# Performance work log

Hardware: AMD Instinct MI355X
Metric: run time of the kernel (lower is better)

The kernel has to match this reference:

```python
import jax, jax.numpy as jnp
import numpy as np

# static sizes
B = 32          # graphs
NPER = 1024     # nodes per graph
N0 = B * NPER
F_IN = 128
H = 4           # heads
DH = 32         # per-head dim (128/4)
HID = H * DH    # 128
E = 524288      # edges (avg degree 16)
K1, K2, K3 = 512, 256, 128  # ceil(0.5*nper) per stage
NC = 10


def gcn_agg(h, src, dst, w, n):
    """GCNConv propagation: sym-normalized aggregation with self-loops.
    h: [n,F] already projected; w: [E] edge weight (0 for filtered edges)."""
    deg = jax.ops.segment_sum(w, dst, num_segments=n) + 1.0  # +1 self-loop
    dinv = jax.lax.rsqrt(deg)
    coef = dinv[src] * dinv[dst] * w                          # [E]
    agg = jax.ops.segment_sum(h[src] * coef[:, None], dst, num_segments=n)
    return agg + h / deg[:, None]  # self-loop term: dinv[i]^2 = 1/deg[i]


def mh_gcn(x, W, b, src, dst, w, n):
    """MAGPoolGCNLayer: per-head GCNConv (32->32), relu, concat heads."""
    h = jnp.einsum('nhd,hde->nhe', x.reshape(n, H, DH), W).reshape(n, HID)
    return jax.nn.relu(gcn_agg(h, src, dst, w, n) + b.reshape(HID))


def att_pool(x, src, dst, w, A, psW, psb, n, k):
    """MultiHeadAtt: standard att, complex score, concat pooling, global weight."""
    sub = x.reshape(n, H, DH)
    att = jnp.einsum('nhd,hd->nh', sub, A)            # per-head Linear(32,1)
    cat = (att[:, :, None] * sub).reshape(n, HID)     # score*sub, concat
    score = (gcn_agg(cat @ psW, src, dst, w, n) + psb)[:, 0]  # GCNConv(HID,1)
    nper = n // B
    _, idx = jax.lax.top_k(score.reshape(B, nper), k)  # per-graph topk
    perm = (idx + jnp.arange(B)[:, None] * nper).reshape(-1)
    xn = x[perm] * jnp.tanh(score[perm])[:, None]      # global att weighting
    # filter_adj: remap kept nodes, mask edges touching dropped nodes
    nmap = jnp.full((n,), -1, jnp.int32).at[perm].set(jnp.arange(B * k, dtype=jnp.int32))
    ns, nd = nmap[src], nmap[dst]
    wn = w * ((ns >= 0) & (nd >= 0)).astype(w.dtype)
    return xn, jnp.maximum(ns, 0), jnp.maximum(nd, 0), wn


def readout(x):
    # graphs are contiguous with equal node counts -> reshape readout
    xr = x.reshape(B, -1, x.shape[-1])
    return jnp.concatenate([xr.max(1), xr.mean(1)], axis=1)  # [B, 2*HID]


def setup_inputs():
    key = jax.random.key(0)
    ks = jax.random.split(key, 26)
    gid = jnp.repeat(jnp.arange(B, dtype=jnp.int32), E // B)
    src = jax.random.randint(ks[0], (E,), 0, NPER, dtype=jnp.int32) + gid * NPER
    dst = jax.random.randint(ks[1], (E,), 0, NPER, dtype=jnp.int32) + gid * NPER
    x = jax.random.normal(ks[2], (N0, F_IN), jnp.float32)
    s = 0.1
    def rn(k, shp):
        return jax.random.normal(k, shp, jnp.float32) * s
    return {
        'x': x, 'src': src, 'dst': dst,
        'W1': rn(ks[3], (H, DH, DH)), 'b1': rn(ks[4], (H, DH)), 'A1': rn(ks[5], (H, DH)),
        'ps1W': rn(ks[6], (HID, 1)), 'ps1b': rn(ks[7], (1,)),
        'W2': rn(ks[8], (H, DH, DH)), 'b2': rn(ks[9], (H, DH)), 'A2': rn(ks[10], (H, DH)),
        'ps2W': rn(ks[11], (HID, 1)), 'ps2b': rn(ks[12], (1,)),
        'W3': rn(ks[13], (H, DH, DH)), 'b3': rn(ks[14], (H, DH)), 'A3': rn(ks[15], (H, DH)),
        'ps3W': rn(ks[16], (HID, 1)), 'ps3b': rn(ks[17], (1,)),
        'l1W': rn(ks[18], (2 * HID, HID)), 'l1b': rn(ks[19], (HID,)),
        'l2W': rn(ks[20], (HID, HID // 2)), 'l2b': rn(ks[21], (HID // 2,)),
        'l3W': rn(ks[22], (HID // 2, NC)), 'l3b': rn(ks[23], (NC,)),
    }


def reference(x, src, dst, W1, b1, A1, ps1W, ps1b, W2, b2, A2, ps2W, ps2b,
              W3, b3, A3, ps3W, ps3b, l1W, l1b, l2W, l2b, l3W, l3b):
    w = jnp.ones((E,), x.dtype)
    h = mh_gcn(x, W1, b1, src, dst, w, N0)
    h, s1, d1, w1 = att_pool(h, src, dst, w, A1, ps1W, ps1b, N0, K1)
    r1 = readout(h)
    n1 = B * K1
    h = mh_gcn(h, W2, b2, s1, d1, w1, n1)
    h, s2, d2, w2 = att_pool(h, s1, d1, w1, A2, ps2W, ps2b, n1, K2)
    r2 = readout(h)
    n2 = B * K2
    h = mh_gcn(h, W3, b3, s2, d2, w2, n2)
    h, _, _, _ = att_pool(h, s2, d2, w2, A3, ps3W, ps3b, n2, K3)
    r3 = readout(h)
    z = r1 + r2 + r3                      # [B, 2*HID]
    z = jax.nn.relu(z @ l1W + l1b)        # dropout skipped (eval mode)
    z = jax.nn.relu(z @ l2W + l2b)
    return jax.nn.log_softmax(z @ l3W + l3b, axis=-1)
```

## Files before the change

### kernel.cpp

```cpp
#include <hip/hip_runtime.h>
#include <math.h>

#define BGR 32
#define NPER0 1024
#define N0 (BGR * NPER0)
#define FDIM 128
#define EDG 524288
#define EPG (EDG / BGR)
#define EBLK (EDG / 256)
#define K1 512
#define K2 256
#define K3 128
#define N1 (BGR * K1)
#define N2 (BGR * K2)
#define SXP 36
#define CAP 64
#define RSEC (BGR * FDIM)

__device__ __forceinline__ unsigned enc_f(float v) {
    unsigned u = __float_as_uint(v);
    return (u & 0x80000000u) ? ~u : (u | 0x80000000u);
}
__device__ __forceinline__ float dec_f(unsigned u) {
    return (u & 0x80000000u) ? __uint_as_float(u ^ 0x80000000u) : __uint_as_float(~u);
}

__device__ __forceinline__ void proj_compute(float* __restrict__ hp, int nb, int t,
                                             const float* __restrict__ sW,
                                             const float* __restrict__ sxT) {
    const int fg = t >> 3, ng = t & 7, h = fg >> 3;
    const float* ap = sxT + h * 32 * SXP + ng * 4;
    const float* bp = sW + h * 1024 + (fg & 7) * 4;
    float4 acc0 = {0.f, 0.f, 0.f, 0.f}, acc1 = acc0, acc2 = acc0, acc3 = acc0;
#pragma unroll
    for (int k = 0; k < 32; k++) {
        float4 a = *(const float4*)(ap + k * SXP);
        float4 b = *(const float4*)(bp + k * 32);
        acc0.x = fmaf(a.x, b.x, acc0.x); acc0.y = fmaf(a.x, b.y, acc0.y);
        acc0.z = fmaf(a.x, b.z, acc0.z); acc0.w = fmaf(a.x, b.w, acc0.w);
        acc1.x = fmaf(a.y, b.x, acc1.x); acc1.y = fmaf(a.y, b.y, acc1.y);
        acc1.z = fmaf(a.y, b.z, acc1.z); acc1.w = fmaf(a.y, b.w, acc1.w);
        acc2.x = fmaf(a.z, b.x, acc2.x); acc2.y = fmaf(a.z, b.y, acc2.y);
        acc2.z = fmaf(a.z, b.z, acc2.z); acc2.w = fmaf(a.z, b.w, acc2.w);
        acc3.x = fmaf(a.w, b.x, acc3.x); acc3.y = fmaf(a.w, b.y, acc3.y);
        acc3.z = fmaf(a.w, b.z, acc3.z); acc3.w = fmaf(a.w, b.w, acc3.w);
    }
    float4* op = (float4*)(hp + (size_t)(nb + ng * 4) * FDIM + fg * 4);
    op[0] = acc0; op[32] = acc1; op[64] = acc2; op[96] = acc3;
}

__device__ __forceinline__ void pool_body(const float* __restrict__ ha,
                                          const int* __restrict__ perm,
                                          const float* __restrict__ mult, int k, int pb,
                                          unsigned* __restrict__ rmax,
                                          float* __restrict__ rsum,
                                          float* __restrict__ smax,
                                          float* __restrict__ ssum) {
    const int t = threadIdx.x;
    const int g = pb & 31;
    const int c = pb >> 5;
    const int f = t & 127, half = t >> 7;
    const int base = g * k + c * 8;
    float vmax = -1e30f, vsum = 0.0f;
#pragma unroll
    for (int j0 = 0; j0 < 4; j0++) {
        int newid = base + half + j0 * 2;
        int old = perm[newid];
        float m = mult[newid];
        float v = ha[(size_t)old * FDIM + f] * m;
        vmax = fmaxf(vmax, v);
        vsum += v;
    }
    if (half) { smax[f] = vmax; ssum[f] = vsum; }
    __syncthreads();
    if (!half) {
        vmax = fmaxf(vmax, smax[f]);
        vsum += ssum[f];
        atomicMax(&rmax[g * FDIM + f], enc_f(vmax));
        atomicAdd(&rsum[g * FDIM + f], vsum);
    }
}

__global__ void bin_proj1(const int* __restrict__ src, const int* __restrict__ dst,
                          int* __restrict__ cnt, int* __restrict__ slot,
                          const float* __restrict__ x, const float* __restrict__ W,
                          float* __restrict__ hp,
                          unsigned* __restrict__ rmax, float* __restrict__ rsum) {
    __shared__ __align__(16) float sW[4096];
    __shared__ __align__(16) float sxT[128 * SXP];
    const int t = threadIdx.x;
    if (blockIdx.x < EBLK) {
        if (blockIdx.x < BGR) {
            int z = blockIdx.x * 256 + t;
            rmax[z] = 0u;
            rsum[z] = 0.0f;
        }
        const int g = blockIdx.x & 31, chunk = blockIdx.x >> 5;
        int e = g * EPG + chunk * 256 + t;
        int s = src[e];
        int d = dst[e];
        int p = atomicAdd(&cnt[d], 1);
        if (p < CAP) slot[(size_t)d * CAP + p] = s;
        return;
    }
    const int tb = blockIdx.x - EBLK;
    const int nb = (tb & 31) * NPER0 + (tb >> 5) * 32;
    for (int i = t; i < 4096; i += 256) sW[i] = W[i];
    for (int i = t; i < 4096; i += 256) {
        int node = i >> 7, dim = i & 127;
        sxT[dim * SXP + node] = x[(size_t)(nb + node) * FDIM + dim];
    }
    __syncthreads();
    proj_compute(hp, nb, t, sW, sxT);
}

__global__ void comp_proj_pool(const int* __restrict__ cnt_prev,
                               const int* __restrict__ slot_prev,
                               const int* __restrict__ nmap,
                               int* __restrict__ cnt_next, int* __restrict__ slot_next,
                               const float* __restrict__ ha, const int* __restrict__ perm,
                               const float* __restrict__ mult, const float* __restrict__ W,
                               float* __restrict__ hp, int ncomp, int ntiles, int kprev,
                               unsigned* __restrict__ rmax, float* __restrict__ rsum) {
    __shared__ __align__(16) float sW[4096];
    __shared__ __align__(16) float sxT[128 * SXP];
    const int t = threadIdx.x;
    if (blockIdx.x < ncomp) {
        const int w = t >> 6, lane = t & 63;
        const int b = (blockIdx.x & 31) * kprev + (blockIdx.x >> 5) * 4 + w;
        const int old = perm[b];
        const int c = min(cnt_prev[old], CAP);
        int a = -1;
        if (lane < c) a = nmap[slot_prev[(size_t)old * CAP + lane]];
        unsigned long long mk = __ballot(a >= 0);
        if (a >= 0) {
            int pos = __popcll(mk & ((1ull << lane) - 1ull));
            slot_next[(size_t)b * CAP + pos] = a;
        }
        if (lane == 0) cnt_next[b] = __popcll(mk);
        return;
    }
    if (blockIdx.x >= ncomp + ntiles) {
        pool_body(ha, perm, mult, kprev, blockIdx.x - (ncomp + ntiles), rmax, rsum,
                  sW, sW + 128);
        return;
    }
    const int tb = blockIdx.x - ncomp;
    const int nb = (tb & 31) * kprev + (tb >> 5) * 32;
    for (int i = t; i < 4096; i += 256) sW[i] = W[i];
    for (int i = t; i < 4096; i += 256) {
        int node = i >> 7, dim = i & 127;
        int newid = nb + node;
        sxT[dim * SXP + node] = ha[(size_t)perm[newid] * FDIM + dim] * mult[newid];
    }
    __syncthreads();
    proj_compute(hp, nb, t, sW, sxT);
}

__global__ void agg_kernel(const float* __restrict__ hp, const float* __restrict__ b,
                           const int* __restrict__ cnt, const int* __restrict__ slot,
                           const float* __restrict__ A, const float* __restrict__ psW,
                           float* __restrict__ ha, float* __restrict__ csd, int nper) {
    const int w = threadIdx.x >> 6;
    const int lane = threadIdx.x & 63;
    const int g = blockIdx.x & 31;
    const int chunk = blockIdx.x >> 5;
    const int i = g * nper + chunk * 4 + w;
    const int ci = cnt[i];
    const float di = rsqrtf((float)ci + 1.0f);
    const int c = min(ci, CAP);
    const float2* __restrict__ hp2 = (const float2*)hp;
    float2 self = hp2[(size_t)i * 64 + lane];
    float accx = self.x * di * di, accy = self.y * di * di;
    int idx = 0;
    float dv = 0.0f;
    if (lane < c) {
        idx = slot[i * CAP + lane];
        dv = rsqrtf((float)cnt[idx] + 1.0f);
    }
    int j = 0;
    for (; j + 3 < c; j += 4) {
        int s0 = __shfl(idx, j, 64);
        int s1 = __shfl(idx, j + 1, 64);
        int s2 = __shfl(idx, j + 2, 64);
        int s3 = __shfl(idx, j + 3, 64);
        float c0 = __shfl(dv, j, 64) * di;
        float c1 = __shfl(dv, j + 1, 64) * di;
        float c2 = __shfl(dv, j + 2, 64) * di;
        float c3 = __shfl(dv, j + 3, 64) * di;
        float2 v0 = hp2[(size_t)s0 * 64 + lane];
        float2 v1 = hp2[(size_t)s1 * 64 + lane];
        float2 v2 = hp2[(size_t)s2 * 64 + lane];
        float2 v3 = hp2[(size_t)s3 * 64 + lane];
        accx = fmaf(v0.x, c0, accx); accy = fmaf(v0.y, c0, accy);
        accx = fmaf(v1.x, c1, accx); accy = fmaf(v1.y, c1, accy);
        accx = fmaf(v2.x, c2, accx); accy = fmaf(v2.y, c2, accy);
        accx = fmaf(v3.x, c3, accx); accy = fmaf(v3.y, c3, accy);
    }
    for (; j < c; j++) {
        int s = __shfl(idx, j, 64);
        float co = __shfl(dv, j, 64) * di;
        float2 v = hp2[(size_t)s * 64 + lane];
        accx = fmaf(v.x, co, accx); accy = fmaf(v.y, co, accy);
    }
    float2 bb = ((const float2*)b)[lane];
    float2 o;
    o.x = fmaxf(accx + bb.x, 0.0f);
    o.y = fmaxf(accy + bb.y, 0.0f);
    ((float2*)ha)[(size_t)i * 64 + lane] = o;
    float2 Av = ((const float2*)A)[lane];
    float2 Pv = ((const float2*)psW)[lane];
    float a = o.x * Av.x + o.y * Av.y;
    float p = o.x * Pv.x + o.y * Pv.y;
#pragma unroll
    for (int d = 8; d > 0; d >>= 1) {
        a += __shfl_down(a, d, 16);
        p += __shfl_down(p, d, 16);
    }
    float part = a * p;
    part += __shfl_down(part, 16, 64);
    part += __shfl_down(part, 32, 64);
    if (lane == 0) csd[i] = part * di;
}

__global__ __launch_bounds__(1024) void topk_kernel(
        const float* __restrict__ csd, const int* __restrict__ cnt,
        const int* __restrict__ slot, const float* __restrict__ psb,
        int nper, int k, int* __restrict__ nmap, int* __restrict__ perm,
        float* __restrict__ mult) {
    __shared__ float cs_l[NPER0];
    __shared__ float sc[NPER0];
    __shared__ unsigned ukey[NPER0];
    __shared__ unsigned hist[256];
    __shared__ unsigned wtot[4];
    __shared__ unsigned sel[2];
    __shared__ int ctr[2];
    const int g = blockIdx.x, t = threadIdx.x;
    const int gnb = g * nper;
    if (t < nper) cs_l[t] = csd[gnb + t];
    if (t == 0) { sel[0] = 0u; sel[1] = (unsigned)k; }
    __syncthreads();
    if (t < nper) {
        int ci = cnt[gnb + t];
        int c = min(ci, CAP);
        const int* srow = slot + (size_t)(gnb + t) * CAP;
        float v = 0.0f;
        for (int j = 0; j < c; j++) v += cs_l[srow[j] - gnb];
        float s = rsqrtf((float)ci + 1.0f) * (v + cs_l[t]) + psb[0];
        sc[t] = s;
        ukey[t] = enc_f(s);
    }
    __syncthreads();
    const int w4 = t >> 6, l = t & 63;
    for (int shift = 24; shift >= 0; shift -= 8) {
        if (t < 256) hist[t] = 0u;
        __syncthreads();
        const unsigned prefix = sel[0];
        const unsigned need = sel[1];
        {
            unsigned u = (t < nper) ? ukey[t] : 0u;
            bool inp = (t < nper) &&
                       ((shift == 24) || ((u >> (shift + 8)) == (prefix >> (shift + 8))));
            int dig = inp ? (int)((u >> shift) & 255u) : -1;
            int cv = inp ? 1 : 0;
#pragma unroll
            for (int d = 1; d < 64; d <<= 1) {
                int od = __shfl_xor(dig, d, 64);
                int oc = __shfl_xor(cv, d, 64);
                if (od == dig) cv = ((l & d) == 0) ? (cv + oc) : 0;
            }
            if (dig >= 0 && cv > 0) atomicAdd(&hist[dig], (unsigned)cv);
        }
        __syncthreads();
        unsigned h = 0, s = 0;
        if (t < 256) {
            h = hist[t];
            s = h;
#pragma unroll
            for (int off = 1; off < 64; off <<= 1) {
                unsigned v2 = __shfl_down(s, off, 64);
                if (l + off < 64) s += v2;
            }
            if (l == 0) wtot[w4] = s;
        }
        __syncthreads();
        if (t < 256) {
            unsigned add = 0;
            for (int ww = w4 + 1; ww < 4; ww++) add += wtot[ww];
            const unsigned sfx = s + add;
            const unsigned gtr = sfx - h;
            if (sfx >= need && gtr < need) {
                sel[0] = prefix | ((unsigned)t << shift);
                sel[1] = need - gtr;
            }
        }
        __syncthreads();
    }
    const unsigned T = sel[0];
    const int need2 = (int)sel[1];
    if (t == 0) { ctr[0] = 0; ctr[1] = k - need2; }
    __syncthreads();
    if (t < nper) {
        unsigned u = ukey[t];
        int newid = -1;
        if (u > T) {
            newid = atomicAdd(&ctr[0], 1);
        } else if (u == T) {
            int s2 = atomicAdd(&ctr[1], 1);
            if (s2 < k) newid = s2;
        }
        nmap[gnb + t] = (newid >= 0) ? g * k + newid : -1;
        if (newid >= 0) {
            perm[g * k + newid] = gnb + t;
            mult[g * k + newid] = tanhf(sc[t]);
        }
    }
}

__global__ __launch_bounds__(1024) void pool3_mlp(
        const float* __restrict__ ha, const int* __restrict__ perm,
        const float* __restrict__ mult,
        const unsigned* __restrict__ rmax, const float* __restrict__ rsum,
        const float* __restrict__ l1W, const float* __restrict__ l1b,
        const float* __restrict__ l2W, const float* __restrict__ l2b,
        const float* __restrict__ l3W, const float* __restrict__ l3b,
        float* __restrict__ out) {
    __shared__ float pm[8][FDIM], ps[8][FDIM];
    __shared__ float sz[256], s1[128], s2[64], s3[16], red[2];
    const int g = blockIdx.x, t = threadIdx.x;
    const int f = t & 127, ch = t >> 7;
    float vmax = -1e30f, vsum = 0.0f;
#pragma unroll
    for (int j = 0; j < K3 / 8; j++) {
        int nid = g * K3 + ch + j * 8;
        int old = perm[nid];
        float m = mult[nid];
        float v = ha[(size_t)old * FDIM + f] * m;
        vmax = fmaxf(vmax, v);
        vsum += v;
    }
    pm[ch][f] = vmax;
    ps[ch][f] = vsum;
    __syncthreads();
    if (t < 128) {
        float M = pm[0][t];
#pragma unroll
        for (int c2 = 1; c2 < 8; c2++) M = fmaxf(M, pm[c2][t]);
        sz[t] = dec_f(rmax[g * FDIM + t]) + dec_f(rmax[RSEC + g * FDIM + t]) + M;
    } else if (t < 256) {
        int f2 = t - 128;
        float S = ps[0][f2];
#pragma unroll
        for (int c2 = 1; c2 < 8; c2++) S += ps[c2][f2];
        sz[t] = rsum[g * FDIM + f2] / (float)K1 + rsum[RSEC + g * FDIM + f2] / (float)K2 +
                S / (float)K3;
    }
    __syncthreads();
    if (t < 128) {
        float acc = l1b[t];
        for (int i = 0; i < 256; i++) acc = fmaf(sz[i], l1W[i * 128 + t], acc);
        s1[t] = fmaxf(acc, 0.0f);
    }
    __syncthreads();
    if (t < 64) {
        float a2 = l2b[t];
        for (int i = 0; i < 128; i++) a2 = fmaf(s1[i], l2W[i * 64 + t], a2);
        s2[t] = fmaxf(a2, 0.0f);
    }
    __syncthreads();
    if (t < 10) {
        float a3 = l3b[t];
        for (int i = 0; i < 64; i++) a3 = fmaf(s2[i], l3W[i * 10 + t], a3);
        s3[t] = a3;
    }
    __syncthreads();
    if (t == 0) {
        float m = -1e30f;
        for (int c = 0; c < 10; c++) m = fmaxf(m, s3[c]);
        float sum = 0.0f;
        for (int c = 0; c < 10; c++) sum += expf(s3[c] - m);
        red[0] = m;
        red[1] = logf(sum);
    }
    __syncthreads();
    if (t < 10) out[g * 10 + t] = s3[t] - red[0] - red[1];
}

extern "C" void kernel_launch(void* const* d_in, const int* in_sizes, int n_in,
                              void* d_out, int out_size, void* d_ws, size_t ws_size,
                              hipStream_t stream) {
    const float* x    = (const float*)d_in[0];
    const int* src0   = (const int*)d_in[1];
    const int* dst0   = (const int*)d_in[2];
    const float* W1   = (const float*)d_in[3];
    const float* b1   = (const float*)d_in[4];
    const float* A1   = (const float*)d_in[5];
    const float* ps1W = (const float*)d_in[6];
    const float* ps1b = (const float*)d_in[7];
    const float* W2   = (const float*)d_in[8];
    const float* b2   = (const float*)d_in[9];
    const float* A2   = (const float*)d_in[10];
    const float* ps2W = (const float*)d_in[11];
    const float* ps2b = (const float*)d_in[12];
    const float* W3   = (const float*)d_in[13];
    const float* b3   = (const float*)d_in[14];
    const float* A3   = (const float*)d_in[15];
    const float* ps3W = (const float*)d_in[16];
    const float* ps3b = (const float*)d_in[17];
    const float* l1W  = (const float*)d_in[18];
    const float* l1b  = (const float*)d_in[19];
    const float* l2W  = (const float*)d_in[20];
    const float* l2b  = (const float*)d_in[21];
    const float* l3W  = (const float*)d_in[22];
    const float* l3b  = (const float*)d_in[23];
    float* out = (float*)d_out;

    char* ws = (char*)d_ws;
    size_t o = 0;
    auto alloc = [&](size_t bytes) -> void* {
        void* p = ws + o;
        o += (bytes + 255) & ~(size_t)255;
        return p;
    };
    float*    hproj = (float*)alloc((size_t)N0 * FDIM * 4);
    float*    hact  = (float*)alloc((size_t)N0 * FDIM * 4);
    int*      cntA  = (int*)alloc(N0 * 4);
    int*      cntB  = (int*)alloc(N1 * 4);
    int*      cntC  = (int*)alloc(N2 * 4);
    int*      slotA = (int*)alloc((size_t)N0 * CAP * 4);
    int*      slotB = (int*)alloc((size_t)N1 * CAP * 4);
    int*      slotC = (int*)alloc((size_t)N2 * CAP * 4);
    float*    cs    = (float*)alloc(N0 * 4);
    int*      nmapA = (int*)alloc(N0 * 4);
    int*      nmapB = (int*)alloc(N1 * 4);
    int*      perm  = (int*)alloc(N1 * 4);
    float*    mult  = (float*)alloc(N1 * 4);
    unsigned* rmax  = (unsigned*)alloc(2 * RSEC * 4);
    float*    rsum  = (float*)alloc(2 * RSEC * 4);

    hipMemsetAsync(cntA, 0, N0 * 4, stream);
    bin_proj1<<<EBLK + N0 / 32, 256, 0, stream>>>(src0, dst0, cntA, slotA, x, W1,
                                                  hproj, rmax, rsum);
    agg_kernel<<<N0 / 4, 256, 0, stream>>>(hproj, b1, cntA, slotA, A1, ps1W, hact, cs, NPER0);
    topk_kernel<<<BGR, 1024, 0, stream>>>(cs, cntA, slotA, ps1b, NPER0, K1,
                                          nmapA, perm, mult);

    comp_proj_pool<<<N1 / 4 + N1 / 32 + BGR * K1 / 8, 256, 0, stream>>>(
        cntA, slotA, nmapA, cntB, slotB, hact, perm, mult, W2, hproj,
        N1 / 4, N1 / 32, K1, rmax, rsum);
    agg_kernel<<<N1 / 4, 256, 0, stream>>>(hproj, b2, cntB, slotB, A2, ps2W, hact, cs, K1);
    topk_kernel<<<BGR, 1024, 0, stream>>>(cs, cntB, slotB, ps2b, K1, K2,
                                          nmapB, perm, mult);

    comp_proj_pool<<<N2 / 4 + N2 / 32 + BGR * K2 / 8, 256, 0, stream>>>(
        cntB, slotB, nmapB, cntC, slotC, hact, perm, mult, W3, hproj,
        N2 / 4, N2 / 32, K2, rmax + RSEC, rsum + RSEC);
    agg_kernel<<<N2 / 4, 256, 0, stream>>>(hproj, b3, cntC, slotC, A3, ps3W, hact, cs, K2);
    topk_kernel<<<BGR, 1024, 0, stream>>>(cs, cntC, slotC, ps3b, K2, K3,
                                          nmapA , perm, mult);

    pool3_mlp<<<BGR, 1024, 0, stream>>>(hact, perm, mult, rmax, rsum,
                                        l1W, l1b, l2W, l2b, l3W, l3b, out);

    (void)in_sizes; (void)n_in; (void)out_size; (void)ws_size;
}
```

Baseline: 247.6 us.

## Aggregate before projecting and fold compaction and pooling into top-k kernel

Uses linearity to run the sparse GCN aggregation on raw features first, then applies the per-head 32x32 projection inside the aggregation kernel. This removes the separate projection pass and its intermediate buffer. Edge compaction, readout pooling and the final MLP now run inside a per-graph top-k kernel with a shared-memory node map, which removes global atomics and several launches. The trade-off is that each aggregation block reloads the 16KB weight matrix, and compaction and pooling now run on only 32 blocks, so there is less parallelism.

```diff
diff --git a/kernel.cpp b/kernel.cpp
--- a/kernel.cpp
+++ b/kernel.cpp
@@ -13,7 +13,6 @@
 #define K3 128
 #define N1 (BGR * K1)
 #define N2 (BGR * K2)
-#define SXP 36
 #define CAP 64
 #define RSEC (BGR * FDIM)
 
@@ -21,193 +20,98 @@
     unsigned u = __float_as_uint(v);
     return (u & 0x80000000u) ? ~u : (u | 0x80000000u);
 }
-__device__ __forceinline__ float dec_f(unsigned u) {
-    return (u & 0x80000000u) ? __uint_as_float(u ^ 0x80000000u) : __uint_as_float(~u);
-}
-
-__device__ __forceinline__ void proj_compute(float* __restrict__ hp, int nb, int t,
-                                             const float* __restrict__ sW,
-                                             const float* __restrict__ sxT) {
-    const int fg = t >> 3, ng = t & 7, h = fg >> 3;
-    const float* ap = sxT + h * 32 * SXP + ng * 4;
-    const float* bp = sW + h * 1024 + (fg & 7) * 4;
-    float4 acc0 = {0.f, 0.f, 0.f, 0.f}, acc1 = acc0, acc2 = acc0, acc3 = acc0;
-#pragma unroll
-    for (int k = 0; k < 32; k++) {
-        float4 a = *(const float4*)(ap + k * SXP);
-        float4 b = *(const float4*)(bp + k * 32);
-        acc0.x = fmaf(a.x, b.x, acc0.x); acc0.y = fmaf(a.x, b.y, acc0.y);
-        acc0.z = fmaf(a.x, b.z, acc0.z); acc0.w = fmaf(a.x, b.w, acc0.w);
-        acc1.x = fmaf(a.y, b.x, acc1.x); acc1.y = fmaf(a.y, b.y, acc1.y);
-        acc1.z = fmaf(a.y, b.z, acc1.z); acc1.w = fmaf(a.y, b.w, acc1.w);
-        acc2.x = fmaf(a.z, b.x, acc2.x); acc2.y = fmaf(a.z, b.y, acc2.y);
-        acc2.z = fmaf(a.z, b.z, acc2.z); acc2.w = fmaf(a.z, b.w, acc2.w);
-        acc3.x = fmaf(a.w, b.x, acc3.x); acc3.y = fmaf(a.w, b.y, acc3.y);
-        acc3.z = fmaf(a.w, b.z, acc3.z); acc3.w = fmaf(a.w, b.w, acc3.w);
-    }
-    float4* op = (float4*)(hp + (size_t)(nb + ng * 4) * FDIM + fg * 4);
-    op[0] = acc0; op[32] = acc1; op[64] = acc2; op[96] = acc3;
-}
-
-__device__ __forceinline__ void pool_body(const float* __restrict__ ha,
-                                          const int* __restrict__ perm,
-                                          const float* __restrict__ mult, int k, int pb,
-                                          unsigned* __restrict__ rmax,
-                                          float* __restrict__ rsum,
-                                          float* __restrict__ smax,
-                                          float* __restrict__ ssum) {
+
+__global__ void bin_kernel(const int* __restrict__ src, const int* __restrict__ dst,
+                           int* __restrict__ cnt, int* __restrict__ slot) {
+    const int g = blockIdx.x & 31, chunk = blockIdx.x >> 5;
+    int e = g * EPG + chunk * 256 + threadIdx.x;
+    int s = src[e];
+    int d = dst[e];
+    int p = atomicAdd(&cnt[d], 1);
+    if (p < CAP) slot[(size_t)d * CAP + p] = s;
+}
+
+__global__ void aggw_kernel(const float* __restrict__ xsrc,
+                            const int* __restrict__ permIn,
+                            const float* __restrict__ multIn,
+                            const int* __restrict__ cnt, const int* __restrict__ slot,
+                            const float* __restrict__ W, const float* __restrict__ b,
+                            const float* __restrict__ A, const float* __restrict__ psW,
+                            float* __restrict__ haOut, float* __restrict__ csd,
+                            int nper) {
+    __shared__ __align__(16) float sW[4096];
+    __shared__ float sY[4][128];
     const int t = threadIdx.x;
-    const int g = pb & 31;
-    const int c = pb >> 5;
-    const int f = t & 127, half = t >> 7;
-    const int base = g * k + c * 8;
-    float vmax = -1e30f, vsum = 0.0f;
-#pragma unroll
-    for (int j0 = 0; j0 < 4; j0++) {
-        int newid = base + half + j0 * 2;
-        int old = perm[newid];
-        float m = mult[newid];
-        float v = ha[(size_t)old * FDIM + f] * m;
-        vmax = fmaxf(vmax, v);
-        vsum += v;
-    }
-    if (half) { smax[f] = vmax; ssum[f] = vsum; }
-    __syncthreads();
-    if (!half) {
-        vmax = fmaxf(vmax, smax[f]);
-        vsum += ssum[f];
-        atomicMax(&rmax[g * FDIM + f], enc_f(vmax));
-        atomicAdd(&rsum[g * FDIM + f], vsum);
-    }
-}
-
-__global__ void bin_proj1(const int* __restrict__ src, const int* __restrict__ dst,
-                          int* __restrict__ cnt, int* __restrict__ slot,
-                          const float* __restrict__ x, const float* __restrict__ W,
-                          float* __restrict__ hp,
-                          unsigned* __restrict__ rmax, float* __restrict__ rsum) {
-    __shared__ __align__(16) float sW[4096];
-    __shared__ __align__(16) float sxT[128 * SXP];
-    const int t = threadIdx.x;
-    if (blockIdx.x < EBLK) {
-        if (blockIdx.x < BGR) {
-            int z = blockIdx.x * 256 + t;
-            rmax[z] = 0u;
-            rsum[z] = 0.0f;
-        }
-        const int g = blockIdx.x & 31, chunk = blockIdx.x >> 5;
-        int e = g * EPG + chunk * 256 + t;
-        int s = src[e];
-        int d = dst[e];
-        int p = atomicAdd(&cnt[d], 1);
-        if (p < CAP) slot[(size_t)d * CAP + p] = s;
-        return;
-    }
-    const int tb = blockIdx.x - EBLK;
-    const int nb = (tb & 31) * NPER0 + (tb >> 5) * 32;
-    for (int i = t; i < 4096; i += 256) sW[i] = W[i];
-    for (int i = t; i < 4096; i += 256) {
-        int node = i >> 7, dim = i & 127;
-        sxT[dim * SXP + node] = x[(size_t)(nb + node) * FDIM + dim];
-    }
-    __syncthreads();
-    proj_compute(hp, nb, t, sW, sxT);
-}
-
-__global__ void comp_proj_pool(const int* __restrict__ cnt_prev,
-                               const int* __restrict__ slot_prev,
-                               const int* __restrict__ nmap,
-                               int* __restrict__ cnt_next, int* __restrict__ slot_next,
-                               const float* __restrict__ ha, const int* __restrict__ perm,
-                               const float* __restrict__ mult, const float* __restrict__ W,
-                               float* __restrict__ hp, int ncomp, int ntiles, int kprev,
-                               unsigned* __restrict__ rmax, float* __restrict__ rsum) {
-    __shared__ __align__(16) float sW[4096];
-    __shared__ __align__(16) float sxT[128 * SXP];
-    const int t = threadIdx.x;
-    if (blockIdx.x < ncomp) {
-        const int w = t >> 6, lane = t & 63;
-        const int b = (blockIdx.x & 31) * kprev + (blockIdx.x >> 5) * 4 + w;
-        const int old = perm[b];
-        const int c = min(cnt_prev[old], CAP);
-        int a = -1;
-        if (lane < c) a = nmap[slot_prev[(size_t)old * CAP + lane]];
-        unsigned long long mk = __ballot(a >= 0);
-        if (a >= 0) {
-            int pos = __popcll(mk & ((1ull << lane) - 1ull));
-            slot_next[(size_t)b * CAP + pos] = a;
-        }
-        if (lane == 0) cnt_next[b] = __popcll(mk);
-        return;
-    }
-    if (blockIdx.x >= ncomp + ntiles) {
-        pool_body(ha, perm, mult, kprev, blockIdx.x - (ncomp + ntiles), rmax, rsum,
-                  sW, sW + 128);
-        return;
-    }
-    const int tb = blockIdx.x - ncomp;
-    const int nb = (tb & 31) * kprev + (tb >> 5) * 32;
-    for (int i = t; i < 4096; i += 256) sW[i] = W[i];
-    for (int i = t; i < 4096; i += 256) {
-        int node = i >> 7, dim = i & 127;
-        int newid = nb + node;
-        sxT[dim * SXP + node] = ha[(size_t)perm[newid] * FDIM + dim] * mult[newid];
-    }
-    __syncthreads();
-    proj_compute(hp, nb, t, sW, sxT);
-}
-
-__global__ void agg_kernel(const float* __restrict__ hp, const float* __restrict__ b,
-                           const int* __restrict__ cnt, const int* __restrict__ slot,
-                           const float* __restrict__ A, const float* __restrict__ psW,
-                           float* __restrict__ ha, float* __restrict__ csd, int nper) {
-    const int w = threadIdx.x >> 6;
-    const int lane = threadIdx.x & 63;
-    const int g = blockIdx.x & 31;
-    const int chunk = blockIdx.x >> 5;
+    const int w = t >> 6, lane = t & 63;
+    const int g = blockIdx.x & 31, chunk = blockIdx.x >> 5;
     const int i = g * nper + chunk * 4 + w;
+    {
+        float4* d4 = (float4*)sW;
+        const float4* s4 = (const float4*)W;
+        for (int q = t; q < 1024; q += 256) d4[q] = s4[q];
+    }
     const int ci = cnt[i];
     const float di = rsqrtf((float)ci + 1.0f);
     const int c = min(ci, CAP);
-    const float2* __restrict__ hp2 = (const float2*)hp;
-    float2 self = hp2[(size_t)i * 64 + lane];
-    float accx = self.x * di * di, accy = self.y * di * di;
-    int idx = 0;
-    float dv = 0.0f;
+    const float2* __restrict__ x2 = (const float2*)xsrc;
+    float selfco = di * di;
+    size_t selfrow = (size_t)i;
+    if (permIn) { selfrow = (size_t)permIn[i]; selfco *= multIn[i]; }
+    float2 self = x2[selfrow * 64 + lane];
+    float accx = self.x * selfco, accy = self.y * selfco;
+    int rowi = 0;
+    float codv = 0.0f;
     if (lane < c) {
-        idx = slot[i * CAP + lane];
-        dv = rsqrtf((float)cnt[idx] + 1.0f);
+        int idx = slot[(size_t)i * CAP + lane];
+        float dv = rsqrtf((float)cnt[idx] + 1.0f);
+        if (permIn) { rowi = permIn[idx]; codv = dv * multIn[idx]; }
+        else        { rowi = idx;         codv = dv; }
     }
     int j = 0;
     for (; j + 3 < c; j += 4) {
-        int s0 = __shfl(idx, j, 64);
-        int s1 = __shfl(idx, j + 1, 64);
-        int s2 = __shfl(idx, j + 2, 64);
-        int s3 = __shfl(idx, j + 3, 64);
-        float c0 = __shfl(dv, j, 64) * di;
-        float c1 = __shfl(dv, j + 1, 64) * di;
-        float c2 = __shfl(dv, j + 2, 64) * di;
-        float c3 = __shfl(dv, j + 3, 64) * di;
-        float2 v0 = hp2[(size_t)s0 * 64 + lane];
-        float2 v1 = hp2[(size_t)s1 * 64 + lane];
-        float2 v2 = hp2[(size_t)s2 * 64 + lane];
-        float2 v3 = hp2[(size_t)s3 * 64 + lane];
+        int s0 = __shfl(rowi, j, 64);
+        int s1 = __shfl(rowi, j + 1, 64);
+        int s2 = __shfl(rowi, j + 2, 64);
+        int s3 = __shfl(rowi, j + 3, 64);
+        float c0 = __shfl(codv, j, 64) * di;
+        float c1 = __shfl(codv, j + 1, 64) * di;
+        float c2 = __shfl(codv, j + 2, 64) * di;
+        float c3 = __shfl(codv, j + 3, 64) * di;
+        float2 v0 = x2[(size_t)s0 * 64 + lane];
+        float2 v1 = x2[(size_t)s1 * 64 + lane];
+        float2 v2 = x2[(size_t)s2 * 64 + lane];
+        float2 v3 = x2[(size_t)s3 * 64 + lane];
         accx = fmaf(v0.x, c0, accx); accy = fmaf(v0.y, c0, accy);
         accx = fmaf(v1.x, c1, accx); accy = fmaf(v1.y, c1, accy);
         accx = fmaf(v2.x, c2, accx); accy = fmaf(v2.y, c2, accy);
         accx = fmaf(v3.x, c3, accx); accy = fmaf(v3.y, c3, accy);
     }
     for (; j < c; j++) {
-        int s = __shfl(idx, j, 64);
-        float co = __shfl(dv, j, 64) * di;
-        float2 v = hp2[(size_t)s * 64 + lane];
+        int s = __shfl(rowi, j, 64);
+        float co = __shfl(codv, j, 64) * di;
+        float2 v = x2[(size_t)s * 64 + lane];
         accx = fmaf(v.x, co, accx); accy = fmaf(v.y, co, accy);
     }
+    sY[w][2 * lane] = accx;
+    sY[w][2 * lane + 1] = accy;
+    __syncthreads();
+    const int f0 = 2 * lane;
+    const int h = f0 >> 5, e0 = f0 & 31;
+    const float* yp = sY[w] + h * 32;
+    const float* wrow = sW + h * 1024 + e0;
     float2 bb = ((const float2*)b)[lane];
+    float ax = bb.x, ay = bb.y;
+#pragma unroll
+    for (int d = 0; d < 32; d++) {
+        float yv = yp[d];
+        float2 wv = *(const float2*)(wrow + d * 32);
+        ax = fmaf(yv, wv.x, ax);
+        ay = fmaf(yv, wv.y, ay);
+    }
     float2 o;
-    o.x = fmaxf(accx + bb.x, 0.0f);
-    o.y = fmaxf(accy + bb.y, 0.0f);
-    ((float2*)ha)[(size_t)i * 64 + lane] = o;
+    o.x = fmaxf(ax, 0.0f);
+    o.y = fmaxf(ay, 0.0f);
+    ((float2*)haOut)[(size_t)i * 64 + lane] = o;
     float2 Av = ((const float2*)A)[lane];
     float2 Pv = ((const float2*)psW)[lane];
     float a = o.x * Av.x + o.y * Av.y;
@@ -223,18 +127,28 @@
     if (lane == 0) csd[i] = part * di;
 }
 
-__global__ __launch_bounds__(1024) void topk_kernel(
+__global__ __launch_bounds__(1024) void tcp_kernel(
         const float* __restrict__ csd, const int* __restrict__ cnt,
         const int* __restrict__ slot, const float* __restrict__ psb,
-        int nper, int k, int* __restrict__ nmap, int* __restrict__ perm,
-        float* __restrict__ mult) {
+        int nper, int k,
+        int* __restrict__ perm, float* __restrict__ mult,
+        int* __restrict__ cntNext, int* __restrict__ slotNext,
+        const float* __restrict__ ha,
+        float* __restrict__ rmaxg, float* __restrict__ rsumg,
+        const float* __restrict__ l1W, const float* __restrict__ l1b,
+        const float* __restrict__ l2W, const float* __restrict__ l2b,
+        const float* __restrict__ l3W, const float* __restrict__ l3b,
+        float* __restrict__ out) {
     __shared__ float cs_l[NPER0];
     __shared__ float sc[NPER0];
     __shared__ unsigned ukey[NPER0];
+    __shared__ int nmap_l[NPER0];
     __shared__ unsigned hist[256];
     __shared__ unsigned wtot[4];
     __shared__ unsigned sel[2];
     __shared__ int ctr[2];
+    __shared__ float pm[8][FDIM], ps[8][FDIM];
+    __shared__ float sz[256], s1[128], s2[64], s3[16], red[2];
     const int g = blockIdx.x, t = threadIdx.x;
     const int gnb = g * nper;
     if (t < nper) cs_l[t] = csd[gnb + t];
@@ -306,53 +220,70 @@
         if (u > T) {
             newid = atomicAdd(&ctr[0], 1);
         } else if (u == T) {
-            int s2 = atomicAdd(&ctr[1], 1);
-            if (s2 < k) newid = s2;
-        }
-        nmap[gnb + t] = (newid >= 0) ? g * k + newid : -1;
+            int s2l = atomicAdd(&ctr[1], 1);
+            if (s2l < k) newid = s2l;
+        }
+        nmap_l[t] = (newid >= 0) ? g * k + newid : -1;
         if (newid >= 0) {
             perm[g * k + newid] = gnb + t;
             mult[g * k + newid] = tanhf(sc[t]);
         }
     }
-}
-
-__global__ __launch_bounds__(1024) void pool3_mlp(
-        const float* __restrict__ ha, const int* __restrict__ perm,
-        const float* __restrict__ mult,
-        const unsigned* __restrict__ rmax, const float* __restrict__ rsum,
-        const float* __restrict__ l1W, const float* __restrict__ l1b,
-        const float* __restrict__ l2W, const float* __restrict__ l2b,
-        const float* __restrict__ l3W, const float* __restrict__ l3b,
-        float* __restrict__ out) {
-    __shared__ float pm[8][FDIM], ps[8][FDIM];
-    __shared__ float sz[256], s1[128], s2[64], s3[16], red[2];
-    const int g = blockIdx.x, t = threadIdx.x;
-    const int f = t & 127, ch = t >> 7;
-    float vmax = -1e30f, vsum = 0.0f;
-#pragma unroll
-    for (int j = 0; j < K3 / 8; j++) {
-        int nid = g * K3 + ch + j * 8;
-        int old = perm[nid];
-        float m = mult[nid];
-        float v = ha[(size_t)old * FDIM + f] * m;
-        vmax = fmaxf(vmax, v);
-        vsum += v;
-    }
-    pm[ch][f] = vmax;
-    ps[ch][f] = vsum;
-    __syncthreads();
-    if (t < 128) {
+    __syncthreads();
+    if (cntNext != nullptr) {
+        const int w16 = t >> 6;
+        for (int bl = w16; bl < k; bl += 16) {
+            const int nb = g * k + bl;
+            const int old = perm[nb];
+            const int c = min(cnt[old], CAP);
+            int a = -1;
+            if (l < c) a = nmap_l[slot[(size_t)old * CAP + l] - gnb];
+            unsigned long long mk = __ballot(a >= 0);
+            if (a >= 0) {
+                int pos = __popcll(mk & ((1ull << l) - 1ull));
+                slotNext[(size_t)nb * CAP + pos] = a;
+            }
+            if (l == 0) cntNext[nb] = __popcll(mk);
+        }
+    }
+    {
+        const int f = t & 127, ch = t >> 7;
+        float vmax = -1e30f, vsum = 0.0f;
+        for (int jj = ch; jj < k; jj += 8) {
+            int nid = g * k + jj;
+            int old = perm[nid];
+            float v = ha[(size_t)old * FDIM + f] * mult[nid];
+            vmax = fmaxf(vmax, v);
+            vsum += v;
+        }
+        pm[ch][f] = vmax;
+        ps[ch][f] = vsum;
+    }
+    __syncthreads();
+    if (out == nullptr) {
+        if (t < FDIM) {
+            float M = pm[0][t], S = ps[0][t];
+#pragma unroll
+            for (int c2 = 1; c2 < 8; c2++) {
+                M = fmaxf(M, pm[c2][t]);
+                S += ps[c2][t];
+            }
+            rmaxg[g * FDIM + t] = M;
+            rsumg[g * FDIM + t] = S;
+        }
+        return;
+    }
+    if (t < FDIM) {
         float M = pm[0][t];
 #pragma unroll
         for (int c2 = 1; c2 < 8; c2++) M = fmaxf(M, pm[c2][t]);
-        sz[t] = dec_f(rmax[g * FDIM + t]) + dec_f(rmax[RSEC + g * FDIM + t]) + M;
+        sz[t] = rmaxg[g * FDIM + t] + rmaxg[RSEC + g * FDIM + t] + M;
     } else if (t < 256) {
         int f2 = t - 128;
         float S = ps[0][f2];
 #pragma unroll
         for (int c2 = 1; c2 < 8; c2++) S += ps[c2][f2];
-        sz[t] = rsum[g * FDIM + f2] / (float)K1 + rsum[RSEC + g * FDIM + f2] / (float)K2 +
+        sz[t] = rsumg[g * FDIM + f2] / (float)K1 + rsumg[RSEC + g * FDIM + f2] / (float)K2 +
                 S / (float)K3;
     }
     __syncthreads();
@@ -422,45 +353,45 @@
         o += (bytes + 255) & ~(size_t)255;
         return p;
     };
-    float*    hproj = (float*)alloc((size_t)N0 * FDIM * 4);
-    float*    hact  = (float*)alloc((size_t)N0 * FDIM * 4);
-    int*      cntA  = (int*)alloc(N0 * 4);
-    int*      cntB  = (int*)alloc(N1 * 4);
-    int*      cntC  = (int*)alloc(N2 * 4);
-    int*      slotA = (int*)alloc((size_t)N0 * CAP * 4);
-    int*      slotB = (int*)alloc((size_t)N1 * CAP * 4);
-    int*      slotC = (int*)alloc((size_t)N2 * CAP * 4);
-    float*    cs    = (float*)alloc(N0 * 4);
-    int*      nmapA = (int*)alloc(N0 * 4);
-    int*      nmapB = (int*)alloc(N1 * 4);
-    int*      perm  = (int*)alloc(N1 * 4);
-    float*    mult  = (float*)alloc(N1 * 4);
-    unsigned* rmax  = (unsigned*)alloc(2 * RSEC * 4);
-    float*    rsum  = (float*)alloc(2 * RSEC * 4);
+    float* ha1   = (float*)alloc((size_t)N0 * FDIM * 4);
+    float* ha2   = (float*)alloc((size_t)N1 * FDIM * 4);
+    float* ha3   = (float*)alloc((size_t)N2 * FDIM * 4);
+    int*   cntA  = (int*)alloc(N0 * 4);
+    int*   cntB  = (int*)alloc(N1 * 4);
+    int*   cntC  = (int*)alloc(N2 * 4);
+    int*   slotA = (int*)alloc((size_t)N0 * CAP * 4);
+    int*   slotB = (int*)alloc((size_t)N1 * CAP * 4);
+    int*   slotC = (int*)alloc((size_t)N2 * CAP * 4);
+    float* cs    = (float*)alloc(N0 * 4);
+    int*   perm  = (int*)alloc(N1 * 4);
+    float* mult  = (float*)alloc(N1 * 4);
+    float* rmaxg = (float*)alloc(2 * RSEC * 4);
+    float* rsumg = (float*)alloc(2 * RSEC * 4);
 
     hipMemsetAsync(cntA, 0, N0 * 4, stream);
-    bin_proj1<<<EBLK + N0 / 32, 256, 0, stream>>>(src0, dst0, cntA, slotA, x, W1,
-                                                  hproj, rmax, rsum);
-    agg_kernel<<<N0 / 4, 256, 0, stream>>>(hproj, b1, cntA, slotA, A1, ps1W, hact, cs, NPER0);
-    topk_kernel<<<BGR, 1024, 0, stream>>>(cs, cntA, slotA, ps1b, NPER0, K1,
-                                          nmapA, perm, mult);
-
-    comp_proj_pool<<<N1 / 4 + N1 / 32 + BGR * K1 / 8, 256, 0, stream>>>(
-        cntA, slotA, nmapA, cntB, slotB, hact, perm, mult, W2, hproj,
-        N1 / 4, N1 / 32, K1, rmax, rsum);
-    agg_kernel<<<N1 / 4, 256, 0, stream>>>(hproj, b2, cntB, slotB, A2, ps2W, hact, cs, K1);
-    topk_kernel<<<BGR, 1024, 0, stream>>>(cs, cntB, slotB, ps2b, K1, K2,
-                                          nmapB, perm, mult);
-
-    comp_proj_pool<<<N2 / 4 + N2 / 32 + BGR * K2 / 8, 256, 0, stream>>>(
-        cntB, slotB, nmapB, cntC, slotC, hact, perm, mult, W3, hproj,
-        N2 / 4, N2 / 32, K2, rmax + RSEC, rsum + RSEC);
-    agg_kernel<<<N2 / 4, 256, 0, stream>>>(hproj, b3, cntC, slotC, A3, ps3W, hact, cs, K2);
-    topk_kernel<<<BGR, 1024, 0, stream>>>(cs, cntC, slotC, ps3b, K2, K3,
-                                          nmapA , perm, mult);
-
-    pool3_mlp<<<BGR, 1024, 0, stream>>>(hact, perm, mult, rmax, rsum,
-                                        l1W, l1b, l2W, l2b, l3W, l3b, out);
+    bin_kernel<<<EBLK, 256, 0, stream>>>(src0, dst0, cntA, slotA);
+    aggw_kernel<<<N0 / 4, 256, 0, stream>>>(x, nullptr, nullptr, cntA, slotA,
+                                            W1, b1, A1, ps1W, ha1, cs, NPER0);
+    tcp_kernel<<<BGR, 1024, 0, stream>>>(cs, cntA, slotA, ps1b, NPER0, K1,
+                                         perm, mult, cntB, slotB, ha1,
+                                         rmaxg, rsumg,
+                                         nullptr, nullptr, nullptr, nullptr,
+                                         nullptr, nullptr, nullptr);
+
+    aggw_kernel<<<N1 / 4, 256, 0, stream>>>(ha1, perm, mult, cntB, slotB,
+                                            W2, b2, A2, ps2W, ha2, cs, K1);
+    tcp_kernel<<<BGR, 1024, 0, stream>>>(cs, cntB, slotB, ps2b, K1, K2,
+                                         perm, mult, cntC, slotC, ha2,
+                                         rmaxg + RSEC, rsumg + RSEC,
+                                         nullptr, nullptr, nullptr, nullptr,
+                                         nullptr, nullptr, nullptr);
+
+    aggw_kernel<<<N2 / 4, 256, 0, stream>>>(ha2, perm, mult, cntC, slotC,
+                                            W3, b3, A3, ps3W, ha3, cs, K2);
+    tcp_kernel<<<BGR, 1024, 0, stream>>>(cs, cntC, slotC, ps3b, K2, K3,
+                                         perm, mult, nullptr, nullptr, ha3,
+                                         rmaxg, rsumg,
+                                         l1W, l1b, l2W, l2b, l3W, l3b, out);
 
     (void)in_sizes; (void)n_in; (void)out_size; (void)ws_size;
 }
```

Measured after the change: 304.1 us. +22.8%, slower.
